# Optimization experiments

Measured on AMD Instinct MI355X. Metric: run time of the kernel, lower is better.

## Reference

```python
import jax, jax.numpy as jnp
import numpy as np


def _grid_sample_bilinear(img, grid):
    # img: [B,C,H,W]; grid: [B,Hg,Wg,2] normalized to [-1,1] (x,y), align_corners=False,
    # zero padding (torch F.grid_sample defaults).
    B, C, H, W = img.shape
    Hg, Wg = grid.shape[1], grid.shape[2]
    gx, gy = grid[..., 0], grid[..., 1]
    ix = (gx + 1.0) * (W * 0.5) - 0.5
    iy = (gy + 1.0) * (H * 0.5) - 0.5
    ix0 = jnp.floor(ix)
    iy0 = jnp.floor(iy)
    tx = (ix - ix0).reshape(B, 1, -1)
    ty = (iy - iy0).reshape(B, 1, -1)
    img_flat = img.reshape(B, C, H * W)

    def corner(xi, yi):
        valid = ((xi >= 0) & (xi < W) & (yi >= 0) & (yi < H)).reshape(B, 1, -1)
        xc = jnp.clip(xi, 0, W - 1).astype(jnp.int32)
        yc = jnp.clip(yi, 0, H - 1).astype(jnp.int32)
        idx = (yc * W + xc).reshape(B, -1)                      # [B, Hg*Wg]
        vals = jax.vmap(lambda f, i: f[:, i])(img_flat, idx)    # [B, C, Hg*Wg]
        return vals * valid

    v00 = corner(ix0, iy0)
    v01 = corner(ix0 + 1, iy0)
    v10 = corner(ix0, iy0 + 1)
    v11 = corner(ix0 + 1, iy0 + 1)
    out = (v00 * (1 - tx) * (1 - ty) + v01 * tx * (1 - ty)
           + v10 * (1 - tx) * ty + v11 * tx * ty)
    return out.reshape(B, C, Hg, Wg)


def setup_inputs() -> dict:
    key = jax.random.key(0)
    ks = jax.random.split(key, 8)
    B, C, RHO, WP = 32, 384, 25, 256
    HC, WC = 64, 64
    D = 2 * C  # 768, channels after polar/cart concat
    std = 0.02
    return {
        "polar_feat": jax.random.normal(ks[0], (B, C, RHO, WP), jnp.float32),
        "cart_feat": jax.random.normal(ks[1], (B, C, HC, WC), jnp.float32),
        "grid": jax.random.uniform(ks[2], (B, RHO, WP, 2), jnp.float32, -1.0, 1.0),
        "W1_0": jax.random.normal(ks[3], (D, 40), jnp.float32) * std,
        "b1_0": jnp.zeros((40,), jnp.float32),
        "W2_0": jax.random.normal(ks[4], (40, 1), jnp.float32) * std,
        "b2_0": jnp.zeros((1,), jnp.float32),
        "W1s": jax.random.normal(ks[5], (24, D + 1, 40), jnp.float32) * std,
        "b1s": jnp.zeros((24, 40), jnp.float32),
        "W2s": jax.random.normal(ks[6], (24, 40, 1), jnp.float32) * std,
        "b2s": jnp.zeros((24, 1), jnp.float32),
    }


def reference(polar_feat, cart_feat, grid, W1_0, b1_0, W2_0, b2_0, W1s, b1s, W2s, b2s):
    # Polar grid-sample fusion of cartesian features onto the polar grid.
    fe_cart_p = _grid_sample_bilinear(cart_feat, grid)              # [B,C,25,Wp]
    fe_cat_p = jnp.concatenate([polar_feat, fe_cart_p], axis=1)     # [B,768,25,Wp]
    # AdaptiveAvgPool2d((None,1)): mean over width.
    fe = jnp.mean(fe_cat_p, axis=3)                                 # [B,768,25]

    feats = jnp.transpose(fe, (2, 0, 1))                            # [25,B,768]
    gelu = lambda x: jax.nn.gelu(x, approximate=False)

    # Head 0: no recurrent input.
    h0 = gelu(feats[0] @ W1_0 + b1_0)
    out0 = h0 @ W2_0 + b2_0                                         # [B,1]

    # Heads 1..24: concat previous scalar output before first linear (fully_local=False).
    def step(out_prev, xs):
        feat, W1, b1, W2, b2 = xs
        x = jnp.concatenate([feat, out_prev], axis=-1)              # [B,769]
        h = gelu(x @ W1 + b1)
        o = h @ W2 + b2                                             # [B,1]
        return o, o

    _, outs = jax.lax.scan(step, out0, (feats[1:], W1s, b1s, W2s, b2s))
    out = jnp.concatenate([out0[None], outs], axis=0)               # [25,B,1]
    out = jnp.transpose(out[:, :, 0], (1, 0))                       # [B,25]
    return jnp.clip(out, 0.0, jnp.pi)
```

## Files before the change

### kernel.cpp

```cpp
#include <hip/hip_runtime.h>
#include <math.h>

#define B_    32
#define C_    384
#define RHO_  25
#define WP_   256
#define PIX_  4096
#define D_    768
#define HID_  40
#define NROWS (B_*C_*RHO_)
#define FE_N (RHO_*B_*D_)

__device__ __forceinline__ float gelu_exact(float x) {
    return 0.5f * x * (1.f + erff(x * 0.70710678118654752f));
}

__global__ __launch_bounds__(256) void prep_kernel(const float* __restrict__ grid,
        const float* __restrict__ W1_0, const float* __restrict__ W1s,
        float* __restrict__ bins, float* __restrict__ W1T, float* __restrict__ fe) {
    __shared__ float lb[PIX_];
    int tid = threadIdx.x;
    if (blockIdx.x < B_ * RHO_) {
        for (int i = tid; i < PIX_ / 4; i += 256) ((float4*)lb)[i] = make_float4(0.f, 0.f, 0.f, 0.f);
        __syncthreads();
        int pt = blockIdx.x * WP_ + tid;
        float2 g = ((const float2*)grid)[pt];
        float ix = (g.x + 1.f) * 32.f - 0.5f;
        float iy = (g.y + 1.f) * 32.f - 0.5f;
        float x0f = floorf(ix), y0f = floorf(iy);
        float fx = ix - x0f, fy = iy - y0f;
        int x0 = (int)x0f, y0 = (int)y0f;
        const float s = 1.f / 256.f;
        if ((unsigned)x0 < 64u) {
            if ((unsigned)y0 < 64u)       atomicAdd(&lb[y0 * 64 + x0],       (1.f - fx) * (1.f - fy) * s);
            if ((unsigned)(y0 + 1) < 64u) atomicAdd(&lb[(y0 + 1) * 64 + x0], (1.f - fx) * fy * s);
        }
        if ((unsigned)(x0 + 1) < 64u) {
            if ((unsigned)y0 < 64u)       atomicAdd(&lb[y0 * 64 + x0 + 1],       fx * (1.f - fy) * s);
            if ((unsigned)(y0 + 1) < 64u) atomicAdd(&lb[(y0 + 1) * 64 + x0 + 1], fx * fy * s);
        }
        __syncthreads();
        float4* dst = (float4*)(bins + (size_t)blockIdx.x * PIX_);
        for (int i = tid; i < PIX_ / 4; i += 256) dst[i] = ((float4*)lb)[i];
    } else if (blockIdx.x < B_ * RHO_ + 25) {
        int i = blockIdx.x - B_ * RHO_;
        const float* src = (i == 0) ? W1_0 : (W1s + (size_t)(i - 1) * 769 * HID_);
        float* dst = W1T + (size_t)i * HID_ * D_;
        for (int idx = tid; idx < HID_ * D_; idx += 256) {
            int j = idx / D_, c = idx % D_;
            dst[idx] = src[c * HID_ + j];
        }
    } else {
        int z = blockIdx.x - (B_ * RHO_ + 25);
        float4* f4 = (float4*)fe;
        int per = FE_N / 4 / 50;
        for (int i = tid; i < per; i += 256)
            f4[z * per + i] = make_float4(0.f, 0.f, 0.f, 0.f);
    }
}

__global__ __launch_bounds__(256) void main_kernel(const float* __restrict__ polar,
        const float* __restrict__ cart, const float* __restrict__ bins,
        float* __restrict__ fe) {
    __shared__ float ldsW[6400];
    int tid = threadIdx.x;
    int lane = tid & 63, w = tid >> 6;
    int o = blockIdx.x >> 3, sub = blockIdx.x & 7;

    if ((o & 3) != 3) {
        int bid = ((o >> 2) * 3 + (o & 3)) * 8 + sub;
        int b   = bid / 96;
        int rem = bid % 96;
        int ct  = rem >> 4;
        int pc  = rem & 15;

        {
            const float4* binb4 = (const float4*)(bins + (size_t)b * RHO_ * PIX_ + pc * 256);
            float4* lw4 = (float4*)ldsW;
            #pragma unroll 2
            for (int i = tid; i < 1600; i += 256) {
                int r = i >> 6, e = i & 63;
                lw4[(r << 6) + e] = binb4[(size_t)r * 1024 + e];
            }
        }
        __syncthreads();

        int j = lane >> 3, q = lane & 7;
        int c0 = ct * 64 + w * 8 + j;
        const float* xp0 = cart + ((size_t)b * C_ + c0) * PIX_ + pc * 256 + q * 4;
        const float* xp1 = xp0 + (size_t)32 * PIX_;

        float acc0[25], acc1[25];
        #pragma unroll
        for (int r = 0; r < 25; ++r) { acc0[r] = 0.f; acc1[r] = 0.f; }

        float4 a0 = *(const float4*)(xp0);
        float4 a1 = *(const float4*)(xp0 + 32);
        float4 b0 = *(const float4*)(xp1);
        float4 b1 = *(const float4*)(xp1 + 32);
        for (int t = 0; t < 8; ++t) {
            float4 xa = a0, xb = b0;
            a0 = a1; b0 = b1;
            if (t < 6) {
                a1 = *(const float4*)(xp0 + (t + 2) * 32);
                b1 = *(const float4*)(xp1 + (t + 2) * 32);
            }
            const float* wb = ldsW + t * 32 + q * 4;
            #pragma unroll
            for (int r = 0; r < 25; ++r) {
                float4 wv = *(const float4*)(wb + (r << 8));
                acc0[r] += xa.x * wv.x + xa.y * wv.y + xa.z * wv.z + xa.w * wv.w;
                acc1[r] += xb.x * wv.x + xb.y * wv.y + xb.z * wv.z + xb.w * wv.w;
            }
        }
        #pragma unroll
        for (int r = 0; r < 25; ++r) {
            acc0[r] += __shfl_xor(acc0[r], 1, 64);
            acc0[r] += __shfl_xor(acc0[r], 2, 64);
            acc0[r] += __shfl_xor(acc0[r], 4, 64);
            acc1[r] += __shfl_xor(acc1[r], 1, 64);
            acc1[r] += __shfl_xor(acc1[r], 2, 64);
            acc1[r] += __shfl_xor(acc1[r], 4, 64);
        }
        if (q == 0) {
            #pragma unroll
            for (int r = 0; r < 25; ++r) {
                float* fr = fe + ((size_t)(r * B_ + b)) * D_ + 384;
                atomicAdd(fr + c0,      acc0[r]);
                atomicAdd(fr + c0 + 32, acc1[r]);
            }
        }
    } else {
        int pid = (o >> 2) * 8 + sub;
        int wid = pid * 4 + w;
        int r0 = wid * 75;
        for (int it = 0; it < 15; ++it) {
            int r = r0 + it * 5;
            float s[5];
            #pragma unroll
            for (int k = 0; k < 5; ++k) {
                float4 v = ((const float4*)(polar + (size_t)(r + k) * WP_))[lane];
                s[k] = v.x + v.y + v.z + v.w;
            }
            #pragma unroll
            for (int m = 32; m >= 1; m >>= 1) {
                #pragma unroll
                for (int k = 0; k < 5; ++k) s[k] += __shfl_xor(s[k], m, 64);
            }
            if (lane == 0) {
                #pragma unroll
                for (int k = 0; k < 5; ++k) {
                    int rr = r + k;
                    int rho = rr % RHO_, cch = (rr / RHO_) % C_, bb = rr / (RHO_ * C_);
                    fe[((size_t)(rho * B_ + bb)) * D_ + cch] = s[k] * (1.f / 256.f);
                }
            }
        }
    }
}

__global__ __launch_bounds__(256) void mlp_pre_kernel(const float* __restrict__ fe,
        const float* __restrict__ W1T, const float* __restrict__ b1_0,
        const float* __restrict__ b1s, float* __restrict__ G) {
    int lane = threadIdx.x & 63;
    int trip = blockIdx.x * 4 + (threadIdx.x >> 6);
    int jh = trip & 1;
    int pair = trip >> 1;
    int i = pair >> 5, b = pair & 31;
    const float4* f4p = (const float4*)(fe + (size_t)(i * B_ + b) * D_);
    float4 f0 = f4p[lane], f1 = f4p[lane + 64], f2 = f4p[lane + 128];
    int j0 = jh * 20;
    #pragma unroll 2
    for (int j = j0; j < j0 + 20; ++j) {
        const float4* w4p = (const float4*)(W1T + ((size_t)i * HID_ + j) * D_);
        float4 w0 = w4p[lane], w1 = w4p[lane + 64], w2 = w4p[lane + 128];
        float s = f0.x*w0.x + f0.y*w0.y + f0.z*w0.z + f0.w*w0.w
                + f1.x*w1.x + f1.y*w1.y + f1.z*w1.z + f1.w*w1.w
                + f2.x*w2.x + f2.y*w2.y + f2.z*w2.z + f2.w*w2.w;
        #pragma unroll
        for (int m = 32; m >= 1; m >>= 1) s += __shfl_xor(s, m, 64);
        if (lane == 0) {
            float bias = (i == 0) ? b1_0[j] : b1s[(i - 1) * HID_ + j];
            G[(size_t)(i * B_ + b) * HID_ + j] = s + bias;
        }
    }
}

__global__ __launch_bounds__(64) void mlp_seq_kernel(const float* __restrict__ G,
        const float* __restrict__ W1s, const float* __restrict__ W2_0,
        const float* __restrict__ b2_0, const float* __restrict__ W2s,
        const float* __restrict__ b2s, float* __restrict__ out) {
    int lane = threadIdx.x;
    int j2 = lane & 31, b = blockIdx.x * 2 + (lane >> 5);
    bool hi = (j2 < 8);
    float g1[25], g2[25], wl1[25], wl2[25], w2a[25], w2b[25], bsc[25];
    #pragma unroll
    for (int i = 0; i < 25; ++i) {
        g1[i] = G[(size_t)(i * B_ + b) * HID_ + j2];
        g2[i] = hi ? G[(size_t)(i * B_ + b) * HID_ + 32 + j2] : 0.f;
    }
    wl1[0] = 0.f; wl2[0] = 0.f;
    w2a[0] = W2_0[j2]; w2b[0] = hi ? W2_0[32 + j2] : 0.f; bsc[0] = b2_0[0];
    #pragma unroll
    for (int i = 1; i < 25; ++i) {
        size_t base = ((size_t)(i - 1) * 769 + 768) * HID_;
        wl1[i] = W1s[base + j2];
        wl2[i] = hi ? W1s[base + 32 + j2] : 0.f;
        w2a[i] = W2s[(i - 1) * HID_ + j2];
        w2b[i] = hi ? W2s[(i - 1) * HID_ + 32 + j2] : 0.f;
        bsc[i] = b2s[i - 1];
    }
    float op = 0.f;
    #pragma unroll
    for (int i = 0; i < 25; ++i) {
        float x1 = g1[i] + op * wl1[i];
        float x2 = g2[i] + op * wl2[i];
        float p = gelu_exact(x1) * w2a[i] + gelu_exact(x2) * w2b[i];
        #pragma unroll
        for (int m = 16; m >= 1; m >>= 1) p += __shfl_xor(p, m, 64);
        float o = p + bsc[i];
        op = o;
        if (j2 == 0) out[b * 25 + i] = fminf(fmaxf(o, 0.f), 3.14159265358979323846f);
    }
}

extern "C" void kernel_launch(void* const* d_in, const int* in_sizes, int n_in,
                              void* d_out, int out_size, void* d_ws, size_t ws_size,
                              hipStream_t stream) {
    const float* polar = (const float*)d_in[0];
    const float* cart  = (const float*)d_in[1];
    const float* grid  = (const float*)d_in[2];
    const float* W1_0  = (const float*)d_in[3];
    const float* b1_0  = (const float*)d_in[4];
    const float* W2_0  = (const float*)d_in[5];
    const float* b2_0  = (const float*)d_in[6];
    const float* W1s   = (const float*)d_in[7];
    const float* b1s   = (const float*)d_in[8];
    const float* W2s   = (const float*)d_in[9];
    const float* b2s   = (const float*)d_in[10];
    float* out = (float*)d_out;

    float* bins = (float*)d_ws;
    float* fe   = bins + (size_t)B_ * RHO_ * PIX_;
    float* G    = fe + (size_t)FE_N;
    float* W1T  = G + (size_t)RHO_ * B_ * HID_;

    prep_kernel<<<B_ * RHO_ + 25 + 50, 256, 0, stream>>>(grid, W1_0, W1s, bins, W1T, fe);
    main_kernel<<<4096, 256, 0, stream>>>(polar, cart, bins, fe);
    mlp_pre_kernel<<<(RHO_ * B_ * 2) / 4, 256, 0, stream>>>(fe, W1T, b1_0, b1s, G);
    mlp_seq_kernel<<<B_ / 2, 64, 0, stream>>>(G, W1s, W2_0, b2_0, W2s, b2s, out);
}
```

Baseline: 213.3 us.

## Split fused polar-mean/cart-sample kernel into two separate launches

The merged main_kernel, which interleaved polar row-mean blocks with cart projection blocks, is replaced by two kernels launched back to back on the same stream. The polar mean now runs as a grid-stride kernel with 2048 blocks, four rows per wave in a strided pattern. The cart kernel keeps the same LDS-weight dot-product scheme. This likely simplifies scheduling and tunes polar memory access, but it gives up the overlap between bandwidth-bound polar reads and compute-heavy cart blocks and adds one launch.

```diff
diff --git a/kernel.cpp b/kernel.cpp
--- a/kernel.cpp
+++ b/kernel.cpp
@@ -10,6 +10,7 @@
 #define HID_  40
 #define NROWS (B_*C_*RHO_)
 #define FE_N (RHO_*B_*D_)
+#define POLARBLK 2048
 
 __device__ __forceinline__ float gelu_exact(float x) {
     return 0.5f * x * (1.f + erff(x * 0.70710678118654752f));
@@ -59,102 +60,103 @@
     }
 }
 
-__global__ __launch_bounds__(256) void main_kernel(const float* __restrict__ polar,
-        const float* __restrict__ cart, const float* __restrict__ bins,
-        float* __restrict__ fe) {
-    __shared__ float ldsW[6400];
-    int tid = threadIdx.x;
-    int lane = tid & 63, w = tid >> 6;
-    int o = blockIdx.x >> 3, sub = blockIdx.x & 7;
-
-    if ((o & 3) != 3) {
-        int bid = ((o >> 2) * 3 + (o & 3)) * 8 + sub;
-        int b   = bid / 96;
-        int rem = bid % 96;
-        int ct  = rem >> 4;
-        int pc  = rem & 15;
-
-        {
-            const float4* binb4 = (const float4*)(bins + (size_t)b * RHO_ * PIX_ + pc * 256);
-            float4* lw4 = (float4*)ldsW;
-            #pragma unroll 2
-            for (int i = tid; i < 1600; i += 256) {
-                int r = i >> 6, e = i & 63;
-                lw4[(r << 6) + e] = binb4[(size_t)r * 1024 + e];
-            }
-        }
-        __syncthreads();
-
-        int j = lane >> 3, q = lane & 7;
-        int c0 = ct * 64 + w * 8 + j;
-        const float* xp0 = cart + ((size_t)b * C_ + c0) * PIX_ + pc * 256 + q * 4;
-        const float* xp1 = xp0 + (size_t)32 * PIX_;
-
-        float acc0[25], acc1[25];
-        #pragma unroll
-        for (int r = 0; r < 25; ++r) { acc0[r] = 0.f; acc1[r] = 0.f; }
-
-        float4 a0 = *(const float4*)(xp0);
-        float4 a1 = *(const float4*)(xp0 + 32);
-        float4 b0 = *(const float4*)(xp1);
-        float4 b1 = *(const float4*)(xp1 + 32);
-        for (int t = 0; t < 8; ++t) {
-            float4 xa = a0, xb = b0;
-            a0 = a1; b0 = b1;
-            if (t < 6) {
-                a1 = *(const float4*)(xp0 + (t + 2) * 32);
-                b1 = *(const float4*)(xp1 + (t + 2) * 32);
-            }
-            const float* wb = ldsW + t * 32 + q * 4;
+__global__ __launch_bounds__(256) void polar_mean_kernel(const float* __restrict__ polar,
+                                                         float* __restrict__ fe) {
+    int wid = blockIdx.x * 4 + (threadIdx.x >> 6);
+    int lane = threadIdx.x & 63;
+    const int NW = POLARBLK * 4;
+    for (int r0 = wid; r0 < NROWS; r0 += 4 * NW) {
+        float s[4];
+        #pragma unroll
+        for (int k = 0; k < 4; ++k) {
+            int r = r0 + k * NW;
+            float4 v = (r < NROWS) ? ((const float4*)(polar + (size_t)r * WP_))[lane]
+                                   : make_float4(0.f, 0.f, 0.f, 0.f);
+            s[k] = v.x + v.y + v.z + v.w;
+        }
+        #pragma unroll
+        for (int m = 32; m >= 1; m >>= 1) {
             #pragma unroll
-            for (int r = 0; r < 25; ++r) {
-                float4 wv = *(const float4*)(wb + (r << 8));
-                acc0[r] += xa.x * wv.x + xa.y * wv.y + xa.z * wv.z + xa.w * wv.w;
-                acc1[r] += xb.x * wv.x + xb.y * wv.y + xb.z * wv.z + xb.w * wv.w;
-            }
-        }
-        #pragma unroll
-        for (int r = 0; r < 25; ++r) {
-            acc0[r] += __shfl_xor(acc0[r], 1, 64);
-            acc0[r] += __shfl_xor(acc0[r], 2, 64);
-            acc0[r] += __shfl_xor(acc0[r], 4, 64);
-            acc1[r] += __shfl_xor(acc1[r], 1, 64);
-            acc1[r] += __shfl_xor(acc1[r], 2, 64);
-            acc1[r] += __shfl_xor(acc1[r], 4, 64);
-        }
-        if (q == 0) {
+            for (int k = 0; k < 4; ++k) s[k] += __shfl_xor(s[k], m, 64);
+        }
+        if (lane == 0) {
             #pragma unroll
-            for (int r = 0; r < 25; ++r) {
-                float* fr = fe + ((size_t)(r * B_ + b)) * D_ + 384;
-                atomicAdd(fr + c0,      acc0[r]);
-                atomicAdd(fr + c0 + 32, acc1[r]);
-            }
-        }
-    } else {
-        int pid = (o >> 2) * 8 + sub;
-        int wid = pid * 4 + w;
-        int r0 = wid * 75;
-        for (int it = 0; it < 15; ++it) {
-            int r = r0 + it * 5;
-            float s[5];
-            #pragma unroll
-            for (int k = 0; k < 5; ++k) {
-                float4 v = ((const float4*)(polar + (size_t)(r + k) * WP_))[lane];
-                s[k] = v.x + v.y + v.z + v.w;
-            }
-            #pragma unroll
-            for (int m = 32; m >= 1; m >>= 1) {
-                #pragma unroll
-                for (int k = 0; k < 5; ++k) s[k] += __shfl_xor(s[k], m, 64);
-            }
-            if (lane == 0) {
-                #pragma unroll
-                for (int k = 0; k < 5; ++k) {
-                    int rr = r + k;
-                    int rho = rr % RHO_, cch = (rr / RHO_) % C_, bb = rr / (RHO_ * C_);
+            for (int k = 0; k < 4; ++k) {
+                int r = r0 + k * NW;
+                if (r < NROWS) {
+                    int rho = r % RHO_, cch = (r / RHO_) % C_, bb = r / (RHO_ * C_);
                     fe[((size_t)(rho * B_ + bb)) * D_ + cch] = s[k] * (1.f / 256.f);
                 }
             }
+        }
+    }
+}
+
+__global__ __launch_bounds__(256) void cart_kernel(const float* __restrict__ cart,
+        const float* __restrict__ bins, float* __restrict__ fe) {
+    __shared__ float ldsW[6400];
+    int tid = threadIdx.x;
+    int bid = blockIdx.x;
+    int b   = bid / 96;
+    int rem = bid % 96;
+    int ct  = rem >> 4;
+    int pc  = rem & 15;
+
+    {
+        const float4* binb4 = (const float4*)(bins + (size_t)b * RHO_ * PIX_ + pc * 256);
+        float4* lw4 = (float4*)ldsW;
+        #pragma unroll 2
+        for (int i = tid; i < 1600; i += 256) {
+            int r = i >> 6, e = i & 63;
+            lw4[(r << 6) + e] = binb4[(size_t)r * 1024 + e];
+        }
+    }
+    __syncthreads();
+
+    int w = tid >> 6, lane = tid & 63;
+    int j = lane >> 3, q = lane & 7;
+    int c0 = ct * 64 + w * 8 + j;
+    const float* xp0 = cart + ((size_t)b * C_ + c0) * PIX_ + pc * 256 + q * 4;
+    const float* xp1 = xp0 + (size_t)32 * PIX_;
+
+    float acc0[25], acc1[25];
+    #pragma unroll
+    for (int r = 0; r < 25; ++r) { acc0[r] = 0.f; acc1[r] = 0.f; }
+
+    float4 a0 = *(const float4*)(xp0);
+    float4 a1 = *(const float4*)(xp0 + 32);
+    float4 b0 = *(const float4*)(xp1);
+    float4 b1 = *(const float4*)(xp1 + 32);
+    for (int t = 0; t < 8; ++t) {
+        float4 xa = a0, xb = b0;
+        a0 = a1; b0 = b1;
+        if (t < 6) {
+            a1 = *(const float4*)(xp0 + (t + 2) * 32);
+            b1 = *(const float4*)(xp1 + (t + 2) * 32);
+        }
+        const float* wb = ldsW + t * 32 + q * 4;
+        #pragma unroll
+        for (int r = 0; r < 25; ++r) {
+            float4 wv = *(const float4*)(wb + (r << 8));
+            acc0[r] += xa.x * wv.x + xa.y * wv.y + xa.z * wv.z + xa.w * wv.w;
+            acc1[r] += xb.x * wv.x + xb.y * wv.y + xb.z * wv.z + xb.w * wv.w;
+        }
+    }
+    #pragma unroll
+    for (int r = 0; r < 25; ++r) {
+        acc0[r] += __shfl_xor(acc0[r], 1, 64);
+        acc0[r] += __shfl_xor(acc0[r], 2, 64);
+        acc0[r] += __shfl_xor(acc0[r], 4, 64);
+        acc1[r] += __shfl_xor(acc1[r], 1, 64);
+        acc1[r] += __shfl_xor(acc1[r], 2, 64);
+        acc1[r] += __shfl_xor(acc1[r], 4, 64);
+    }
+    if (q == 0) {
+        #pragma unroll
+        for (int r = 0; r < 25; ++r) {
+            float* fr = fe + ((size_t)(r * B_ + b)) * D_ + 384;
+            atomicAdd(fr + c0,      acc0[r]);
+            atomicAdd(fr + c0 + 32, acc1[r]);
         }
     }
 }
@@ -246,7 +248,8 @@
     float* W1T  = G + (size_t)RHO_ * B_ * HID_;
 
     prep_kernel<<<B_ * RHO_ + 25 + 50, 256, 0, stream>>>(grid, W1_0, W1s, bins, W1T, fe);
-    main_kernel<<<4096, 256, 0, stream>>>(polar, cart, bins, fe);
+    polar_mean_kernel<<<POLARBLK, 256, 0, stream>>>(polar, fe);
+    cart_kernel<<<B_ * 6 * 16, 256, 0, stream>>>(cart, bins, fe);
     mlp_pre_kernel<<<(RHO_ * B_ * 2) / 4, 256, 0, stream>>>(fe, W1T, b1_0, b1s, G);
     mlp_seq_kernel<<<B_ / 2, 64, 0, stream>>>(G, W1s, W2_0, b2_0, W2s, b2s, out);
 }
```

Measured after the change: 205.4 us. 1.04x faster.
